# Kernel optimization log

Hardware: AMD Instinct MI355X
Metric: run time of the kernel (lower is better)

## Reference

```python
import jax, jax.numpy as jnp
from jax import lax
import numpy as np

N, B_GRAPHS, E = 50000, 64, 800000
NODE_DIM, HID, HEADS, NUM_CLASSES = 128, 32, 4, 10
EPS_BN = 1e-5


def setup_inputs() -> dict:
    key = jax.random.key(0)
    ks = jax.random.split(key, 32)
    s = 0.08
    HH = HID * HEADS  # 128
    d = {}
    d['x'] = jax.random.normal(ks[0], (N, NODE_DIM), jnp.float32)
    d['edgeIndex'] = jax.random.randint(ks[1], (2, E), 0, N, dtype=jnp.int32)
    d['batch'] = jnp.sort(jax.random.randint(ks[2], (N,), 0, B_GRAPHS, dtype=jnp.int32))
    # GAT layer 0: nodeDim -> HID x HEADS (concat)
    d['W0'] = jax.random.normal(ks[3], (NODE_DIM, HH), jnp.float32) * s
    d['a0s'] = jax.random.normal(ks[4], (HEADS, HID), jnp.float32) * s
    d['a0d'] = jax.random.normal(ks[5], (HEADS, HID), jnp.float32) * s
    d['b0'] = jnp.zeros((HH,), jnp.float32)
    # GAT layer 1: HH -> HID x HEADS (concat)
    d['W1'] = jax.random.normal(ks[6], (HH, HH), jnp.float32) * s
    d['a1s'] = jax.random.normal(ks[7], (HEADS, HID), jnp.float32) * s
    d['a1d'] = jax.random.normal(ks[8], (HEADS, HID), jnp.float32) * s
    d['b1'] = jnp.zeros((HH,), jnp.float32)
    # GAT layer 2: HH -> HID, heads=1, concat=False
    d['W2'] = jax.random.normal(ks[9], (HH, HID), jnp.float32) * s
    d['a2s'] = jax.random.normal(ks[10], (1, HID), jnp.float32) * s
    d['a2d'] = jax.random.normal(ks[11], (1, HID), jnp.float32) * s
    d['b2'] = jnp.zeros((HID,), jnp.float32)
    # BatchNorm (eval mode, running_mean=0, running_var=1) after layers 0,1
    d['g0'] = jnp.ones((HH,), jnp.float32); d['be0'] = jnp.zeros((HH,), jnp.float32)
    d['g1'] = jnp.ones((HH,), jnp.float32); d['be1'] = jnp.zeros((HH,), jnp.float32)
    # post Conv1d stack: 1 -> HID -> HID//2, kernel 5, pad 2
    d['c0w'] = jax.random.normal(ks[12], (HID, 1, 5), jnp.float32) * s
    d['c0b'] = jnp.zeros((HID,), jnp.float32)
    d['cg0'] = jnp.ones((HID,), jnp.float32); d['cb0'] = jnp.zeros((HID,), jnp.float32)
    d['c1w'] = jax.random.normal(ks[13], (HID // 2, HID, 5), jnp.float32) * s
    d['c1b'] = jnp.zeros((HID // 2,), jnp.float32)
    # classifier: (HID//2) -> (HID//4) -> numClasses
    d['l1w'] = jax.random.normal(ks[14], (HID // 2, HID // 4), jnp.float32) * s
    d['l1b'] = jnp.zeros((HID // 4,), jnp.float32)
    d['l2w'] = jax.random.normal(ks[15], (HID // 4, NUM_CLASSES), jnp.float32) * s
    d['l2b'] = jnp.zeros((NUM_CLASSES,), jnp.float32)
    return d


def _gat(x, src, dst, W, a_s, a_d, b, concat):
    Nn = x.shape[0]
    H, O = a_s.shape
    h = (x @ W).reshape(Nn, H, O)               # (N,H,O)
    es = (h * a_s[None]).sum(-1)                # (N,H)
    ed = (h * a_d[None]).sum(-1)
    e = jax.nn.leaky_relu(es[src] + ed[dst], 0.2)  # (E,H)
    m = jax.ops.segment_max(e, dst, num_segments=Nn)
    w = jnp.exp(e - m[dst])
    den = jax.ops.segment_sum(w, dst, num_segments=Nn)
    alpha = w / (den[dst] + 1e-16)              # edge softmax per dst node
    out = jax.ops.segment_sum(h[src] * alpha[:, :, None], dst, num_segments=Nn)
    out = out.reshape(Nn, H * O) if concat else out.mean(axis=1)
    return out + b


def _bn_eval(x, g, b):
    # eval-mode BatchNorm1d with running_mean=0, running_var=1
    return g * x * (1.0 / jnp.sqrt(1.0 + EPS_BN)) + b


def _conv1d(x, w, b):
    y = lax.conv_general_dilated(x, w, (1,), [(2, 2)], dimension_numbers=('NCH', 'OIH', 'NCH'))
    return y + b[None, :, None]


def reference(x, edgeIndex, batch, W0, a0s, a0d, b0, W1, a1s, a1d, b1, W2, a2s, a2d, b2,
              g0, be0, g1, be1, c0w, c0b, cg0, cb0, c1w, c1b, l1w, l1b, l2w, l2b):
    loops = jnp.arange(N, dtype=edgeIndex.dtype)
    src = jnp.concatenate([edgeIndex[0], loops])   # PyG GATConv adds self-loops
    dst = jnp.concatenate([edgeIndex[1], loops])
    elu = jax.nn.elu  # alp = 1.0
    # layer 0
    h0 = _gat(x.astype(jnp.float32), src, dst, W0, a0s, a0d, b0, True)
    h0 = elu(_bn_eval(h0, g0, be0))                # dropout inactive in eval
    # layer 1 (+ residual, shapes match)
    h1 = _gat(h0, src, dst, W1, a1s, a1d, b1, True) + h0
    h1 = elu(_bn_eval(h1, g1, be1))
    # layer 2 (last: no norm/act, no residual -- shape changes)
    h2 = _gat(h1, src, dst, W2, a2s, a2d, b2, False)  # (N, HID)
    # global mean pool over graphs
    sums = jax.ops.segment_sum(h2, batch, num_segments=B_GRAPHS)
    cnt = jax.ops.segment_sum(jnp.ones((N,), jnp.float32), batch, num_segments=B_GRAPHS)
    pooled = sums / jnp.maximum(cnt, 1.0)[:, None]    # (B, HID)
    # post 1D conv stack
    z = pooled[:, None, :]                            # (B,1,HID)
    z = _conv1d(z, c0w, c0b)
    z = elu(cg0[None, :, None] * z * (1.0 / jnp.sqrt(1.0 + EPS_BN)) + cb0[None, :, None])
    z = _conv1d(z, c1w, c1b)                          # (B, HID//2, HID)
    z = z.mean(axis=-1)                               # adaptive avg pool -> (B, HID//2)
    embed = z
    logits = elu(z @ l1w + l1b) @ l2w + l2b
    return jax.nn.log_softmax(logits, axis=-1), embed
```

## Files before the change

### kernel.cpp

```cpp
#include <hip/hip_runtime.h>
#include <hip/hip_bf16.h>


#define NNODES 50000
#define NEDGES 800000
#define BN_INV 0.9999950000374997f
#define SCAN_NB 49

typedef __attribute__((ext_vector_type(8))) short bf16x8;
typedef __attribute__((ext_vector_type(4))) float f32x4;
typedef __attribute__((ext_vector_type(2))) float f32x2;

__device__ __forceinline__ unsigned bf16rne(float f) {
  unsigned u = __float_as_uint(f);
  return (u + 0x7fffu + ((u >> 16) & 1u)) >> 16;
}
__device__ __forceinline__ float bf_lo(unsigned u) { return __uint_as_float(u << 16); }
__device__ __forceinline__ float bf_hi(unsigned u) { return __uint_as_float(u & 0xffff0000u); }

__device__ __forceinline__ unsigned char fp8enc(float f) {
  return (unsigned char)(__builtin_amdgcn_cvt_pk_fp8_f32(f, f, 0u, false) & 0xffu);
}


__global__ __launch_bounds__(256) void count_deg(const int* __restrict__ dst,
                                                 int* __restrict__ deg, int E) {
  int i = blockIdx.x * 256 + threadIdx.x;
  if (i < E) atomicAdd(&deg[dst[i]], 1);
}

__global__ __launch_bounds__(1024) void scan_local(const int* __restrict__ deg,
    int* __restrict__ loc, int* __restrict__ bsum, int Nn) {
  __shared__ int wsum[16];
  __shared__ int woff[17];
  int b = blockIdx.x, t = threadIdx.x, lane = t & 63, w = t >> 6;
  int i = b * 1024 + t;
  int v = (i < Nn) ? deg[i] : 0;
  int incl = v;
#pragma unroll
  for (int o = 1; o < 64; o <<= 1) { int x = __shfl_up(incl, o); if (lane >= o) incl += x; }
  if (lane == 63) wsum[w] = incl;
  __syncthreads();
  if (t == 0) {
    int r = 0;
#pragma unroll
    for (int j = 0; j < 16; ++j) { woff[j] = r; r += wsum[j]; }
    bsum[b] = r;
  }
  __syncthreads();
  if (i < Nn) loc[i] = woff[w] + incl - v;
}

__global__ __launch_bounds__(1024) void scan_finish(const int* __restrict__ loc,
    const int* __restrict__ bsum, int* __restrict__ offs, int* __restrict__ cursor,
    int Nn, int nb) {
  __shared__ int boff[65];
  int b = blockIdx.x, t = threadIdx.x;
  if (t < 64) {
    int v = (t < nb) ? bsum[t] : 0;
    int incl = v;
#pragma unroll
    for (int o = 1; o < 64; o <<= 1) { int x = __shfl_up(incl, o); if (t >= o) incl += x; }
    boff[t + 1] = incl;
    if (t == 0) boff[0] = 0;
  }
  __syncthreads();
  int base = boff[b];
  int i = b * 1024 + t;
  if (i < Nn) { int o = loc[i] + base; offs[i] = o; cursor[i] = o; }
  if (b == 0 && t == 0) offs[Nn] = boff[nb];
}

__global__ __launch_bounds__(256) void fill_csr(const int* __restrict__ src,
    const int* __restrict__ dst, int* __restrict__ cursor,
    int* __restrict__ csr, int E) {
  int i = blockIdx.x * 256 + threadIdx.x;
  if (i < E) {
    int d = dst[i];
    int pos = atomicAdd(&cursor[d], 1);
    csr[pos] = src[i];
  }
}


__global__ __launch_bounds__(256) void prep_kernel(
    const float* __restrict__ W0, const float* __restrict__ W1, const float* __restrict__ W2,
    const float* __restrict__ a0s, const float* __restrict__ a0d,
    const float* __restrict__ a1s, const float* __restrict__ a1d,
    const float* __restrict__ a2s, const float* __restrict__ a2d,
    unsigned short* __restrict__ W0t, unsigned short* __restrict__ W1t,
    unsigned short* __restrict__ W2t,
    float* __restrict__ u0s, float* __restrict__ u0d,
    float* __restrict__ u1s, float* __restrict__ u1d,
    float* __restrict__ u2s, float* __restrict__ u2d) {
  int b = blockIdx.x, t = threadIdx.x;
  if (b < 64) {
    int idx = b * 256 + t; int c = idx >> 7, k = idx & 127;
    W0t[idx] = (unsigned short)bf16rne(W0[k * 128 + c]);
  } else if (b < 128) {
    int idx = (b - 64) * 256 + t; int c = idx >> 7, k = idx & 127;
    W1t[idx] = (unsigned short)bf16rne(W1[k * 128 + c]);
  } else if (b < 144) {
    int idx = (b - 128) * 256 + t; int c = idx >> 7, k = idx & 127;
    W2t[idx] = (unsigned short)bf16rne(W2[k * 32 + c]);
  } else if (b == 144) {
    for (int it = 0; it < 4; ++it) {
      int idx = it * 256 + t;
      int k = idx >> 3, rem = idx & 7, h = rem >> 1, sd = rem & 1;
      const float* av = sd ? a0d : a0s;
      float s = 0.f;
      for (int o = 0; o < 32; ++o) s += W0[k * 128 + h * 32 + o] * av[h * 32 + o];
      (sd ? u0d : u0s)[k * 4 + h] = s;
    }
  } else if (b == 145) {
    for (int it = 0; it < 4; ++it) {
      int idx = it * 256 + t;
      int k = idx >> 3, rem = idx & 7, h = rem >> 1, sd = rem & 1;
      const float* av = sd ? a1d : a1s;
      float s = 0.f;
      for (int o = 0; o < 32; ++o) s += W1[k * 128 + h * 32 + o] * av[h * 32 + o];
      (sd ? u1d : u1s)[k * 4 + h] = s;
    }
  } else {
    int k = t >> 1, sd = t & 1;
    const float* av = sd ? a2d : a2s;
    float s = 0.f;
    for (int o = 0; o < 32; ++o) s += W2[k * 32 + o] * av[o];
    (sd ? u2d : u2s)[k] = s;
  }
}


__global__ __launch_bounds__(256) void xprep_kernel(const float* __restrict__ x,
    unsigned* __restrict__ xbf, const float* __restrict__ u0s,
    const float* __restrict__ u0d, float* __restrict__ es, float* __restrict__ ed,
    int Nn) {
  int n = blockIdx.x * 4 + (threadIdx.x >> 6);
  if (n >= Nn) return;
  int l = threadIdx.x & 63;
  int c0 = 2 * l;
  float2 v = *(const float2*)&x[(size_t)n * 128 + c0];
  xbf[(size_t)n * 64 + l] = bf16rne(v.x) | (bf16rne(v.y) << 16);
  float ps[4], pd[4];
#pragma unroll
  for (int h = 0; h < 4; ++h) {
    ps[h] = v.x * u0s[c0 * 4 + h] + v.y * u0s[(c0 + 1) * 4 + h];
    pd[h] = v.x * u0d[c0 * 4 + h] + v.y * u0d[(c0 + 1) * 4 + h];
  }
#pragma unroll
  for (int h = 0; h < 4; ++h)
#pragma unroll
    for (int o = 32; o; o >>= 1) { ps[h] += __shfl_xor(ps[h], o); pd[h] += __shfl_xor(pd[h], o); }
  if (l == 0) {
#pragma unroll
    for (int h = 0; h < 4; ++h) { es[n * 4 + h] = ps[h]; ed[n * 4 + h] = pd[h]; }
  }
}


template <int NC>
__global__ __launch_bounds__(256) void gemm_mfma(const unsigned short* __restrict__ Abf,
    const unsigned short* __restrict__ Wt, unsigned char* __restrict__ Hfp,
    int Nrows) {
  constexpr int NT = NC / 16;
  __shared__ unsigned short lw[NC][136];
  int tid = threadIdx.x;
  for (int idx = tid; idx < NC * 16; idx += 256) {
    int c = idx >> 4, k0 = (idx & 15) * 8;
    *(uint4*)&lw[c][k0] = *(const uint4*)&Wt[c * 128 + k0];
  }
  __syncthreads();
  int w = tid >> 6, l = tid & 63;
  int g = l >> 4, i = l & 15;
  int rbase = blockIdx.x * 64 + w * 16;
  int arow = rbase + i; arow = arow < Nrows ? arow : Nrows - 1;
  bf16x8 a[4];
#pragma unroll
  for (int kk = 0; kk < 4; ++kk)
    a[kk] = *(const bf16x8*)&Abf[(size_t)arow * 128 + kk * 32 + g * 8];
  f32x4 acc[NT];
#pragma unroll
  for (int t = 0; t < NT; ++t) acc[t] = (f32x4){0.f, 0.f, 0.f, 0.f};
#pragma unroll
  for (int kk = 0; kk < 4; ++kk) {
#pragma unroll
    for (int t = 0; t < NT; ++t) {
      bf16x8 b = *(const bf16x8*)&lw[t * 16 + i][kk * 32 + g * 8];
      acc[t] = __builtin_amdgcn_mfma_f32_16x16x32_bf16(a[kk], b, acc[t], 0, 0, 0);
    }
  }
  int crow0 = rbase + g * 4;
#pragma unroll
  for (int t = 0; t < NT; ++t)
#pragma unroll
    for (int r = 0; r < 4; ++r) {
      int row = crow0 + r;
      if (row < Nrows)
        Hfp[(size_t)row * NC + t * 16 + i] = fp8enc(acc[t][r]);
    }
}


template <bool RES, bool WRITE_F32, int NEXT_NH>
__global__ __launch_bounds__(256) void gat_agg128(const uint2* __restrict__ hfp,
    const float* __restrict__ es, const float* __restrict__ ed,
    const int* __restrict__ offs, const int* __restrict__ csr,
    const float* __restrict__ bias, const float* __restrict__ gamma,
    const float* __restrict__ beta, const float* __restrict__ resid,
    float* __restrict__ out_f32, uint4* __restrict__ out_bf,
    const float* __restrict__ uns, const float* __restrict__ und,
    float* __restrict__ es_next, float* __restrict__ ed_next, int Nn) {
  constexpr int CHK = 16;
  int tid = threadIdx.x;
  int l = tid & 63;
  int q = l & 15;
  int n = blockIdx.x * 16 + (tid >> 6) * 4 + (l >> 4);
  if (n >= Nn) return;
  int hh = q >> 2;
  unsigned c0 = q * 8;
  float edn = ed[n * 4 + hh];
  float e0 = es[n * 4 + hh] + edn;
  e0 = e0 > 0.f ? e0 : 0.2f * e0;
  float w0 = __expf(e0);
  float den = w0;
  float acc[8];
  {
    uint2 u = hfp[(unsigned)n * 16 + q];
    f32x2 p0 = __builtin_amdgcn_cvt_pk_f32_fp8(u.x, false);
    f32x2 p1 = __builtin_amdgcn_cvt_pk_f32_fp8(u.x, true);
    f32x2 p2 = __builtin_amdgcn_cvt_pk_f32_fp8(u.y, false);
    f32x2 p3 = __builtin_amdgcn_cvt_pk_f32_fp8(u.y, true);
    acc[0] = w0 * p0.x; acc[1] = w0 * p0.y;
    acc[2] = w0 * p1.x; acc[3] = w0 * p1.y;
    acc[4] = w0 * p2.x; acc[5] = w0 * p2.y;
    acc[6] = w0 * p3.x; acc[7] = w0 * p3.y;
  }
  int beg = offs[n], end = offs[n + 1];
  for (int base = beg; base < end; base += CHK) {
    int cnt = end - base;
    int s[CHK];
#pragma unroll
    for (int j = 0; j < CHK; ++j) s[j] = (j < cnt) ? csr[base + j] : n;
    uint2 hv[CHK];
#pragma unroll
    for (int j = 0; j < CHK; ++j) hv[j] = hfp[(unsigned)s[j] * 16 + q];
    float w[CHK];
#pragma unroll
    for (int j = 0; j < CHK; ++j) {
      float e = es[s[j] * 4 + hh] + edn;
      e = e > 0.f ? e : 0.2f * e;
      w[j] = (j < cnt) ? __expf(e) : 0.f;
    }
#pragma unroll
    for (int j = 0; j < CHK; ++j) {
      f32x2 p0 = __builtin_amdgcn_cvt_pk_f32_fp8(hv[j].x, false);
      f32x2 p1 = __builtin_amdgcn_cvt_pk_f32_fp8(hv[j].x, true);
      f32x2 p2 = __builtin_amdgcn_cvt_pk_f32_fp8(hv[j].y, false);
      f32x2 p3 = __builtin_amdgcn_cvt_pk_f32_fp8(hv[j].y, true);
      den += w[j];
      acc[0] += w[j] * p0.x; acc[1] += w[j] * p0.y;
      acc[2] += w[j] * p1.x; acc[3] += w[j] * p1.y;
      acc[4] += w[j] * p2.x; acc[5] += w[j] * p2.y;
      acc[6] += w[j] * p3.x; acc[7] += w[j] * p3.y;
    }
  }
  float inv = 1.0f / (den + 1e-16f);
  f32x4 bi0 = *(const f32x4*)&bias[c0],  bi1 = *(const f32x4*)&bias[c0 + 4];
  f32x4 ga0 = *(const f32x4*)&gamma[c0], ga1 = *(const f32x4*)&gamma[c0 + 4];
  f32x4 be0 = *(const f32x4*)&beta[c0],  be1 = *(const f32x4*)&beta[c0 + 4];
  f32x4 r0 = (f32x4){0.f,0.f,0.f,0.f}, r1 = r0;
  if (RES) {
    r0 = *(const f32x4*)&resid[(size_t)n * 128 + c0];
    r1 = *(const f32x4*)&resid[(size_t)n * 128 + c0 + 4];
  }
  float o[8];
#pragma unroll
  for (int k = 0; k < 8; ++k) {
    float bi = k < 4 ? bi0[k] : bi1[k - 4];
    float ga = k < 4 ? ga0[k] : ga1[k - 4];
    float be = k < 4 ? be0[k] : be1[k - 4];
    float rv = k < 4 ? r0[k] : r1[k - 4];
    float v = acc[k] * inv + bi;
    if (RES) v += rv;
    v = ga * v * BN_INV + be;
    o[k] = v > 0.f ? v : __expf(v) - 1.f;
  }
  if (WRITE_F32) {
    f32x4 f0 = {o[0], o[1], o[2], o[3]}, f1 = {o[4], o[5], o[6], o[7]};
    *(f32x4*)&out_f32[(size_t)n * 128 + c0] = f0;
    *(f32x4*)&out_f32[(size_t)n * 128 + c0 + 4] = f1;
  }
  uint4 p;
  p.x = bf16rne(o[0]) | (bf16rne(o[1]) << 16);
  p.y = bf16rne(o[2]) | (bf16rne(o[3]) << 16);
  p.z = bf16rne(o[4]) | (bf16rne(o[5]) << 16);
  p.w = bf16rne(o[6]) | (bf16rne(o[7]) << 16);
  out_bf[(unsigned)n * 16 + q] = p;
  if (NEXT_NH == 4) {
    const f32x4* uns4 = (const f32x4*)uns;
    const f32x4* und4 = (const f32x4*)und;
    f32x4 ps = (f32x4){0.f,0.f,0.f,0.f}, pd = ps;
#pragma unroll
    for (int k = 0; k < 8; ++k) {
      f32x4 us = uns4[c0 + k], ud = und4[c0 + k];
#pragma unroll
      for (int h = 0; h < 4; ++h) { ps[h] += o[k] * us[h]; pd[h] += o[k] * ud[h]; }
    }
#pragma unroll
    for (int h = 0; h < 4; ++h)
#pragma unroll
      for (int m = 1; m < 16; m <<= 1) {
        ps[h] += __shfl_xor(ps[h], m);
        pd[h] += __shfl_xor(pd[h], m);
      }
    if (q == 0) {
#pragma unroll
      for (int h = 0; h < 4; ++h) {
        es_next[n * 4 + h] = ps[h];
        ed_next[n * 4 + h] = pd[h];
      }
    }
  } else {
    float ps = 0.f, pd = 0.f;
#pragma unroll
    for (int k = 0; k < 8; ++k) { ps += o[k] * uns[c0 + k]; pd += o[k] * und[c0 + k]; }
#pragma unroll
    for (int m = 1; m < 16; m <<= 1) { ps += __shfl_xor(ps, m); pd += __shfl_xor(pd, m); }
    if (q == 0) { es_next[n] = ps; ed_next[n] = pd; }
  }
}


__global__ __launch_bounds__(256) void gat_agg32(const unsigned short* __restrict__ hfp,
    const float* __restrict__ es, const float* __restrict__ ed,
    const int* __restrict__ offs, const int* __restrict__ csr,
    const float* __restrict__ bias, float* __restrict__ h2, int Nn) {
  constexpr int CHK = 16;
  int tid = threadIdx.x;
  int l = tid & 63;
  int q = l & 15;
  int n = blockIdx.x * 16 + (tid >> 6) * 4 + (l >> 4);
  if (n >= Nn) return;
  float edn = ed[n];
  float e0 = es[n] + edn;
  e0 = e0 > 0.f ? e0 : 0.2f * e0;
  float w0 = __expf(e0);
  float den = w0;
  float accx, accy;
  {
    f32x2 p = __builtin_amdgcn_cvt_pk_f32_fp8((unsigned)hfp[(unsigned)n * 16 + q], false);
    accx = w0 * p.x; accy = w0 * p.y;
  }
  int beg = offs[n], end = offs[n + 1];
  for (int base = beg; base < end; base += CHK) {
    int cnt = end - base;
    int s[CHK];
#pragma unroll
    for (int j = 0; j < CHK; ++j) s[j] = (j < cnt) ? csr[base + j] : n;
    unsigned short u[CHK];
#pragma unroll
    for (int j = 0; j < CHK; ++j) u[j] = hfp[(unsigned)s[j] * 16 + q];
    float w[CHK];
#pragma unroll
    for (int j = 0; j < CHK; ++j) {
      float e = es[s[j]] + edn;
      e = e > 0.f ? e : 0.2f * e;
      w[j] = (j < cnt) ? __expf(e) : 0.f;
    }
#pragma unroll
    for (int j = 0; j < CHK; ++j) {
      f32x2 p = __builtin_amdgcn_cvt_pk_f32_fp8((unsigned)u[j], false);
      den += w[j];
      accx += w[j] * p.x;
      accy += w[j] * p.y;
    }
  }
  float inv = 1.0f / (den + 1e-16f);
  float2 bi = *(const float2*)&bias[2 * q];
  float2 o;
  o.x = accx * inv + bi.x;
  o.y = accy * inv + bi.y;
  *(float2*)&h2[(size_t)n * 32 + 2 * q] = o;
}


__global__ __launch_bounds__(256) void head_kernel(const float* __restrict__ h2,
    const int* __restrict__ batch,
    const float* __restrict__ c0w, const float* __restrict__ c0b,
    const float* __restrict__ cg0, const float* __restrict__ cb0,
    const float* __restrict__ c1w, const float* __restrict__ c1b,
    const float* __restrict__ l1w, const float* __restrict__ l1b,
    const float* __restrict__ l2w, const float* __restrict__ l2b,
    float* __restrict__ out) {
  int b = blockIdx.x;
  int t = threadIdx.x;
  __shared__ float sums[8][32];
  __shared__ float pooled[32];
  __shared__ float z1[32][32];
  __shared__ float z2[16][32];
  __shared__ float emb[16];
  __shared__ float hfc[8];
  __shared__ float logits[10];

  int lo = 0, hi = NNODES;
  while (lo < hi) { int mid = (lo + hi) >> 1; if (batch[mid] < b) lo = mid + 1; else hi = mid; }
  int start = lo;
  lo = 0; hi = NNODES;
  while (lo < hi) { int mid = (lo + hi) >> 1; if (batch[mid] < b + 1) lo = mid + 1; else hi = mid; }
  int end = lo;

  {
    int ch = t & 31, g = t >> 5;
    float s = 0.f;
    for (int i = start + g; i < end; i += 8) s += h2[(size_t)i * 32 + ch];
    sums[g][ch] = s;
  }
  __syncthreads();
  if (t < 32) {
    float s = 0.f;
#pragma unroll
    for (int g = 0; g < 8; ++g) s += sums[g][t];
    float cn = fmaxf((float)(end - start), 1.0f);
    pooled[t] = s / cn;
  }
  __syncthreads();
  for (int i = t; i < 1024; i += 256) {
    int oc = i >> 5, tt = i & 31;
    float a = c0b[oc];
#pragma unroll
    for (int k = 0; k < 5; ++k) {
      int p = tt + k - 2;
      if (p >= 0 && p < 32) a += pooled[p] * c0w[oc * 5 + k];
    }
    a = cg0[oc] * a * BN_INV + cb0[oc];
    z1[oc][tt] = a > 0.f ? a : __expf(a) - 1.f;
  }
  __syncthreads();
  for (int i = t; i < 512; i += 256) {
    int oc = i >> 5, tt = i & 31;
    float a = c1b[oc];
    for (int ic = 0; ic < 32; ++ic) {
      const float* wrow = &c1w[(oc * 32 + ic) * 5];
#pragma unroll
      for (int k = 0; k < 5; ++k) {
        int p = tt + k - 2;
        if (p >= 0 && p < 32) a += z1[ic][p] * wrow[k];
      }
    }
    z2[oc][tt] = a;
  }
  __syncthreads();
  if (t < 16) {
    float s = 0.f;
    for (int i = 0; i < 32; ++i) s += z2[t][i];
    s *= (1.0f / 32.0f);
    emb[t] = s;
    out[640 + b * 16 + t] = s;
  }
  __syncthreads();
  if (t < 8) {
    float a = l1b[t];
    for (int i = 0; i < 16; ++i) a += emb[i] * l1w[i * 8 + t];
    hfc[t] = a > 0.f ? a : __expf(a) - 1.f;
  }
  __syncthreads();
  if (t < 10) {
    float a = l2b[t];
    for (int j = 0; j < 8; ++j) a += hfc[j] * l2w[j * 10 + t];
    logits[t] = a;
  }
  __syncthreads();
  if (t == 0) {
    float m = logits[0];
    for (int k = 1; k < 10; ++k) m = fmaxf(m, logits[k]);
    float s = 0.f;
    for (int k = 0; k < 10; ++k) s += __expf(logits[k] - m);
    float lse = m + logf(s);
    for (int k = 0; k < 10; ++k) out[b * 10 + k] = logits[k] - lse;
  }
}


extern "C" void kernel_launch(void* const* d_in, const int* in_sizes, int n_in,
                              void* d_out, int out_size, void* d_ws, size_t ws_size,
                              hipStream_t stream) {
  const float* x   = (const float*)d_in[0];
  const int* eidx  = (const int*)d_in[1];
  const int* esrc  = eidx;
  const int* edst  = eidx + NEDGES;
  const int* batch = (const int*)d_in[2];
  const float* W0  = (const float*)d_in[3];
  const float* a0s = (const float*)d_in[4];
  const float* a0d = (const float*)d_in[5];
  const float* b0  = (const float*)d_in[6];
  const float* W1  = (const float*)d_in[7];
  const float* a1s = (const float*)d_in[8];
  const float* a1d = (const float*)d_in[9];
  const float* b1  = (const float*)d_in[10];
  const float* W2  = (const float*)d_in[11];
  const float* a2s = (const float*)d_in[12];
  const float* a2d = (const float*)d_in[13];
  const float* b2  = (const float*)d_in[14];
  const float* g0  = (const float*)d_in[15];
  const float* be0 = (const float*)d_in[16];
  const float* g1  = (const float*)d_in[17];
  const float* be1 = (const float*)d_in[18];
  const float* c0w = (const float*)d_in[19];
  const float* c0b = (const float*)d_in[20];
  const float* cg0 = (const float*)d_in[21];
  const float* cb0 = (const float*)d_in[22];
  const float* c1w = (const float*)d_in[23];
  const float* c1b = (const float*)d_in[24];
  const float* l1w = (const float*)d_in[25];
  const float* l1b = (const float*)d_in[26];
  const float* l2w = (const float*)d_in[27];
  const float* l2b = (const float*)d_in[28];

  char* ws = (char*)d_ws;
  int*            deg    = (int*)(ws + 0);
  int*            cursor = (int*)(ws + 208448);
  int*            offs   = (int*)(ws + 408448);
  float*          esA    = (float*)(ws + 608512);
  float*          edA    = (float*)(ws + 1408512);
  float*          esB    = (float*)(ws + 2208512);
  float*          edB    = (float*)(ws + 3008512);
  int*            csr    = (int*)(ws + 3808512);
  unsigned*       Abf    = (unsigned*)(ws + 7008512);
  unsigned char*  hfp    = (unsigned char*)(ws + 19808512);
  float*          act0   = (float*)(ws + 32608512);
  unsigned short* W0t    = (unsigned short*)(ws + 58208512);
  unsigned short* W1t    = (unsigned short*)(ws + 58241280);
  unsigned short* W2t    = (unsigned short*)(ws + 58274048);
  float*          u0s    = (float*)(ws + 58282240);
  float*          u0d    = (float*)(ws + 58284288);
  float*          u1s    = (float*)(ws + 58286336);
  float*          u1d    = (float*)(ws + 58288384);
  float*          u2s    = (float*)(ws + 58290432);
  float*          u2d    = (float*)(ws + 58290944);
  int*            sloc   = (int*)(ws + 58291456);
  int*            sbsum  = (int*)(ws + 58491456);
  float*          h2     = act0;
  float*          out    = (float*)d_out;

  hipMemsetAsync(d_ws, 0, 200000, stream);

  count_deg<<<(NEDGES + 255) / 256, 256, 0, stream>>>(edst, deg, NEDGES);
  scan_local<<<SCAN_NB, 1024, 0, stream>>>(deg, sloc, sbsum, NNODES);
  scan_finish<<<SCAN_NB, 1024, 0, stream>>>(sloc, sbsum, offs, cursor, NNODES, SCAN_NB);
  fill_csr<<<(NEDGES + 255) / 256, 256, 0, stream>>>(esrc, edst, cursor, csr, NEDGES);

  prep_kernel<<<147, 256, 0, stream>>>(W0, W1, W2, a0s, a0d, a1s, a1d, a2s, a2d,
                                       W0t, W1t, W2t, u0s, u0d, u1s, u1d, u2s, u2d);
  xprep_kernel<<<NNODES / 4, 256, 0, stream>>>(x, Abf, u0s, u0d, esA, edA, NNODES);

  const int ggrid = (NNODES + 63) / 64;
  const int agrid = (NNODES + 15) / 16;

  gemm_mfma<128><<<ggrid, 256, 0, stream>>>((const unsigned short*)Abf, W0t,
                                            hfp, NNODES);
  gat_agg128<false, true, 4><<<agrid, 256, 0, stream>>>(
      (const uint2*)hfp, esA, edA, offs, csr, b0, g0, be0, nullptr,
      act0, (uint4*)Abf, u1s, u1d, esB, edB, NNODES);

  gemm_mfma<128><<<ggrid, 256, 0, stream>>>((const unsigned short*)Abf, W1t,
                                            hfp, NNODES);
  gat_agg128<true, false, 1><<<agrid, 256, 0, stream>>>(
      (const uint2*)hfp, esB, edB, offs, csr, b1, g1, be1, act0,
      nullptr, (uint4*)Abf, u2s, u2d, esA, edA, NNODES);

  gemm_mfma<32><<<ggrid, 256, 0, stream>>>((const unsigned short*)Abf, W2t,
                                           hfp, NNODES);
  gat_agg32<<<agrid, 256, 0, stream>>>((const unsigned short*)hfp,
                                       esA, edA, offs, csr, b2, h2, NNODES);

  head_kernel<<<64, 256, 0, stream>>>(h2, batch, c0w, c0b, cg0, cb0,
                                      c1w, c1b, l1w, l1b, l2w, l2b, out);
}
```

Measured before the change: 332.3 us.

## Sort nodes by degree to balance wavefront work in GAT aggregation

After: 533.3 us. 60.5% more time.

```diff
diff --git a/kernel.cpp b/kernel.cpp
--- a/kernel.cpp
+++ b/kernel.cpp
@@ -79,6 +79,33 @@
     int d = dst[i];
     int pos = atomicAdd(&cursor[d], 1);
     csr[pos] = src[i];
+  }
+}
+
+
+__global__ __launch_bounds__(256) void hist_deg(const int* __restrict__ deg,
+                                                int* __restrict__ hist, int Nn) {
+  int i = blockIdx.x * 256 + threadIdx.x;
+  if (i < Nn) atomicAdd(&hist[min(deg[i], 63)], 1);
+}
+
+__global__ __launch_bounds__(64) void scan_hist(const int* __restrict__ hist,
+                                                int* __restrict__ bincur) {
+  int t = threadIdx.x;
+  int v = hist[t];
+  int incl = v;
+#pragma unroll
+  for (int o = 1; o < 64; o <<= 1) { int x = __shfl_up(incl, o); if (t >= o) incl += x; }
+  bincur[t] = incl - v;
+}
+
+__global__ __launch_bounds__(256) void scatter_perm(const int* __restrict__ deg,
+    int* __restrict__ bincur, int* __restrict__ perm, int Nn) {
+  int i = blockIdx.x * 256 + threadIdx.x;
+  if (i < Nn) {
+    int b = min(deg[i], 63);
+    int pos = atomicAdd(&bincur[b], 1);
+    perm[pos] = i;
   }
 }
 
@@ -205,17 +232,19 @@
 __global__ __launch_bounds__(256) void gat_agg128(const uint2* __restrict__ hfp,
     const float* __restrict__ es, const float* __restrict__ ed,
     const int* __restrict__ offs, const int* __restrict__ csr,
+    const int* __restrict__ perm,
     const float* __restrict__ bias, const float* __restrict__ gamma,
     const float* __restrict__ beta, const float* __restrict__ resid,
     float* __restrict__ out_f32, uint4* __restrict__ out_bf,
     const float* __restrict__ uns, const float* __restrict__ und,
     float* __restrict__ es_next, float* __restrict__ ed_next, int Nn) {
-  constexpr int CHK = 16;
+  constexpr int CHK = 8;
   int tid = threadIdx.x;
   int l = tid & 63;
   int q = l & 15;
-  int n = blockIdx.x * 16 + (tid >> 6) * 4 + (l >> 4);
-  if (n >= Nn) return;
+  int nid = blockIdx.x * 16 + (tid >> 6) * 4 + (l >> 4);
+  if (nid >= Nn) return;
+  int n = perm[nid];
   int hh = q >> 2;
   unsigned c0 = q * 8;
   float edn = ed[n * 4 + hh];
@@ -334,13 +363,15 @@
 __global__ __launch_bounds__(256) void gat_agg32(const unsigned short* __restrict__ hfp,
     const float* __restrict__ es, const float* __restrict__ ed,
     const int* __restrict__ offs, const int* __restrict__ csr,
+    const int* __restrict__ perm,
     const float* __restrict__ bias, float* __restrict__ h2, int Nn) {
-  constexpr int CHK = 16;
+  constexpr int CHK = 8;
   int tid = threadIdx.x;
   int l = tid & 63;
   int q = l & 15;
-  int n = blockIdx.x * 16 + (tid >> 6) * 4 + (l >> 4);
-  if (n >= Nn) return;
+  int nid = blockIdx.x * 16 + (tid >> 6) * 4 + (l >> 4);
+  if (nid >= Nn) return;
+  int n = perm[nid];
   float edn = ed[n];
   float e0 = es[n] + edn;
   e0 = e0 > 0.f ? e0 : 0.2f * e0;
@@ -518,6 +549,8 @@
 
   char* ws = (char*)d_ws;
   int*            deg    = (int*)(ws + 0);
+  int*            hist   = (int*)(ws + 200000);
+  int*            bincur = (int*)(ws + 200256);
   int*            cursor = (int*)(ws + 208448);
   int*            offs   = (int*)(ws + 408448);
   float*          esA    = (float*)(ws + 608512);
@@ -539,14 +572,18 @@
   float*          u2d    = (float*)(ws + 58290944);
   int*            sloc   = (int*)(ws + 58291456);
   int*            sbsum  = (int*)(ws + 58491456);
+  int*            perm   = (int*)(ws + 58491712);
   float*          h2     = act0;
   float*          out    = (float*)d_out;
 
-  hipMemsetAsync(d_ws, 0, 200000, stream);
+  hipMemsetAsync(d_ws, 0, 200512, stream);
 
   count_deg<<<(NEDGES + 255) / 256, 256, 0, stream>>>(edst, deg, NEDGES);
   scan_local<<<SCAN_NB, 1024, 0, stream>>>(deg, sloc, sbsum, NNODES);
   scan_finish<<<SCAN_NB, 1024, 0, stream>>>(sloc, sbsum, offs, cursor, NNODES, SCAN_NB);
+  hist_deg<<<(NNODES + 255) / 256, 256, 0, stream>>>(deg, hist, NNODES);
+  scan_hist<<<1, 64, 0, stream>>>(hist, bincur);
+  scatter_perm<<<(NNODES + 255) / 256, 256, 0, stream>>>(deg, bincur, perm, NNODES);
   fill_csr<<<(NEDGES + 255) / 256, 256, 0, stream>>>(esrc, edst, cursor, csr, NEDGES);
 
   prep_kernel<<<147, 256, 0, stream>>>(W0, W1, W2, a0s, a0d, a1s, a1d, a2s, a2d,
@@ -559,19 +596,19 @@
   gemm_mfma<128><<<ggrid, 256, 0, stream>>>((const unsigned short*)Abf, W0t,
                                             hfp, NNODES);
   gat_agg128<false, true, 4><<<agrid, 256, 0, stream>>>(
-      (const uint2*)hfp, esA, edA, offs, csr, b0, g0, be0, nullptr,
+      (const uint2*)hfp, esA, edA, offs, csr, perm, b0, g0, be0, nullptr,
       act0, (uint4*)Abf, u1s, u1d, esB, edB, NNODES);
 
   gemm_mfma<128><<<ggrid, 256, 0, stream>>>((const unsigned short*)Abf, W1t,
                                             hfp, NNODES);
   gat_agg128<true, false, 1><<<agrid, 256, 0, stream>>>(
-      (const uint2*)hfp, esB, edB, offs, csr, b1, g1, be1, act0,
+      (const uint2*)hfp, esB, edB, offs, csr, perm, b1, g1, be1, act0,
       nullptr, (uint4*)Abf, u2s, u2d, esA, edA, NNODES);
 
   gemm_mfma<32><<<ggrid, 256, 0, stream>>>((const unsigned short*)Abf, W2t,
                                            hfp, NNODES);
   gat_agg32<<<agrid, 256, 0, stream>>>((const unsigned short*)hfp,
-                                       esA, edA, offs, csr, b2, h2, NNODES);
+                                       esA, edA, offs, csr, perm, b2, h2, NNODES);
 
   head_kernel<<<64, 256, 0, stream>>>(h2, batch, c0w, c0b, cg0, cb0,
                                       c1w, c1b, l1w, l1b, l2w, l2b, out);
```
